# Kernel optimization log

Hardware: AMD Instinct MI355X
Metric: run time of the kernel (lower is better)

## Reference

```python
import jax, jax.numpy as jnp
import numpy as np

B, N, S, F = 16384, 1152, 576, 8  # batch, n_sites, n_symm, features
LOG2 = float(np.log(2.0))


def log_cosh(x):
    # numerically stable log(cosh(x)) = |x| + log1p(exp(-2|x|)) - log(2)
    a = jnp.abs(x)
    return a + jnp.log1p(jnp.exp(-2.0 * a)) - LOG2


def setup_inputs() -> dict:
    key = jax.random.key(0)
    ks = iter(jax.random.split(key, 32))
    f32 = jnp.float32
    d = {}
    d['x'] = jax.random.normal(next(ks), (B, N), dtype=f32)
    d['symmetries'] = jax.random.randint(next(ks), (S, N), 0, N, dtype=jnp.int32)
    d['corr0'] = jax.random.randint(next(ks), (576, 4), 0, N, dtype=jnp.int32)
    d['corr1'] = jax.random.randint(next(ks), (576, 4), 0, N, dtype=jnp.int32)
    d['corr2'] = jax.random.randint(next(ks), (24, 24), 0, N, dtype=jnp.int32)
    d['corr3'] = jax.random.randint(next(ks), (24, 24), 0, N, dtype=jnp.int32)
    d['corr0_symm'] = jax.random.randint(next(ks), (S, 576), 0, 576, dtype=jnp.int32)
    d['corr1_symm'] = jax.random.randint(next(ks), (S, 576), 0, 576, dtype=jnp.int32)
    d['corr2_symm'] = jax.random.randint(next(ks), (S, 24), 0, 24, dtype=jnp.int32)
    d['corr3_symm'] = jax.random.randint(next(ks), (S, 24), 0, 24, dtype=jnp.int32)
    std = 0.01
    d['hidden_bias'] = std * jax.random.normal(next(ks), (F,), dtype=f32)
    d['symm_kernel'] = std * jax.random.normal(next(ks), (F, N), dtype=f32)
    d['visible_bias'] = std * jax.random.normal(next(ks), (2,), dtype=f32)
    d['corr0_bias'] = std * jax.random.normal(next(ks), (1,), dtype=f32)
    d['corr0_kernel'] = std * jax.random.normal(next(ks), (F, 576), dtype=f32)
    d['corr1_bias'] = std * jax.random.normal(next(ks), (1,), dtype=f32)
    d['corr1_kernel'] = std * jax.random.normal(next(ks), (F, 576), dtype=f32)
    d['corr2_bias'] = std * jax.random.normal(next(ks), (1,), dtype=f32)
    d['corr2_kernel'] = std * jax.random.normal(next(ks), (F, 24), dtype=f32)
    d['corr3_bias'] = std * jax.random.normal(next(ks), (1,), dtype=f32)
    d['corr3_kernel'] = std * jax.random.normal(next(ks), (F, 24), dtype=f32)
    d['loop0_hidden_bias'] = std * jax.random.normal(next(ks), (F,), dtype=f32)
    d['loop0_kernel'] = std * jax.random.normal(next(ks), (F, 24), dtype=f32)
    d['loop1_hidden_bias'] = std * jax.random.normal(next(ks), (F,), dtype=f32)
    d['loop1_kernel'] = std * jax.random.normal(next(ks), (F, 24), dtype=f32)
    return d


def reference(x, symmetries, corr0, corr1, corr2, corr3,
              corr0_symm, corr1_symm, corr2_symm, corr3_symm,
              hidden_bias, symm_kernel, visible_bias,
              corr0_bias, corr0_kernel, corr1_bias, corr1_kernel,
              corr2_bias, corr2_kernel, corr3_bias, corr3_kernel,
              loop0_hidden_bias, loop0_kernel, loop1_hidden_bias, loop1_kernel):
    n_batch = x.shape[0]
    # symmetrized kernel: (F, S, N)
    K = jnp.take(symm_kernel, symmetries, axis=1)
    theta = jnp.einsum('bn,fsn->bfs', x, K)  # (B, F, S)
    theta = theta + hidden_bias[:, None]
    bias = jnp.sum(x.reshape(n_batch, -1, 2), axis=1) @ visible_bias  # (B,)

    correlators = [corr0, corr1, corr2, corr3]
    corr_symms = [corr0_symm, corr1_symm, corr2_symm, corr3_symm]
    corr_biases = [corr0_bias, corr1_bias, corr2_bias, corr3_bias]
    corr_kernels = [corr0_kernel, corr1_kernel, corr2_kernel, corr3_kernel]

    corr_values = []
    for corr, csym, cb, ck in zip(correlators, corr_symms, corr_biases, corr_kernels):
        ckk = jnp.take(ck, csym, axis=1)               # (F, S, C)
        cv = jnp.take(x, corr, axis=1).prod(axis=2)    # (B, C)
        corr_values.append(cv)
        theta = theta + jnp.einsum('bc,fsc->bfs', cv, ckk)
        bias = bias + cb * jnp.sum(cv, axis=1)

    out = jnp.sum(log_cosh(theta), axis=(1, 2))  # (B,)

    # last two correlators are loop correlators with dedicated hidden units
    loop_params = [(loop0_hidden_bias, loop0_kernel, corr2_symm, corr_values[2]),
                   (loop1_hidden_bias, loop1_kernel, corr3_symm, corr_values[3])]
    for lhb, lk, lsym, lv in loop_params:
        lkk = jnp.take(lk, lsym, axis=1)                      # (F, S, C)
        lt = jnp.einsum('bc,fsc->bfs', lv, lkk) + lhb[:, None]
        out = out + jnp.sum(log_cosh(lt), axis=(1, 2))

    return out + bias
```

## Files before the change

kernel.cpp:

```cpp
#include <hip/hip_runtime.h>
#include <math.h>

#define B_    16384
#define N_    1152
#define KPAD  2560
#define NK32  80
#define KLOOP 256
#define NOUT  4608
#define NT2   18
#define LOG2F_ 0.69314718055994530942f

typedef unsigned short ushort_t;
typedef __attribute__((ext_vector_type(8))) short short8;
typedef __attribute__((ext_vector_type(4))) float floatx4;

__device__ __forceinline__ float log_cosh_f(float t) {
    float a = fabsf(t);
    return a + __logf(1.0f + __expf(-2.0f * a)) - LOG2F_;
}
__device__ __forceinline__ ushort_t bf16_rne(float f) {
    unsigned int u = __float_as_uint(f);
    return (ushort_t)((u + 0x7fffu + ((u >> 16) & 1u)) >> 16);
}
__device__ __forceinline__ float bf16_to_f(ushort_t h) {
    return __uint_as_float(((unsigned int)h) << 16);
}

typedef __attribute__((address_space(1))) const unsigned int guint;
typedef __attribute__((address_space(3))) unsigned int luint;
__device__ __forceinline__ void gload16(const ushort_t* src, ushort_t* dst) {
    __builtin_amdgcn_global_load_lds((guint*)src, (luint*)dst, 16, 0, 0);
}

#define PIPE_WAIT(N) do {                                     \
    asm volatile("s_waitcnt vmcnt(" #N ")" ::: "memory");     \
    __builtin_amdgcn_s_barrier();                             \
    asm volatile("" ::: "memory"); } while (0)

__global__ __launch_bounds__(256) void build_w(
    const int* __restrict__ symm,
    const int* __restrict__ c0s, const int* __restrict__ c1s,
    const int* __restrict__ c2s, const int* __restrict__ c3s,
    const float* __restrict__ sk,
    const float* __restrict__ ck0, const float* __restrict__ ck1,
    const float* __restrict__ ck2, const float* __restrict__ ck3,
    const float* __restrict__ l0k, const float* __restrict__ l1k,
    ushort_t* __restrict__ Wb, ushort_t* __restrict__ LWb)
{
    __shared__ int idx[2352];
    const int s = blockIdx.x;
    const int tid = threadIdx.x;
    for (int i = tid; i < 1152; i += 256) idx[i] = symm[s * N_ + i];
    for (int i = tid; i < 576; i += 256) idx[1152 + i] = c0s[s * 576 + i];
    for (int i = tid; i < 576; i += 256) idx[1728 + i] = c1s[s * 576 + i];
    if (tid < 24) idx[2304 + tid] = c2s[s * 24 + tid];
    else if (tid < 48) idx[2328 + (tid - 24)] = c3s[s * 24 + (tid - 24)];
    __syncthreads();
    for (int f = 0; f < 8; ++f) {
        ushort_t* wr = Wb + (size_t)(s * 8 + f) * KPAD;
        for (int k = tid; k < KPAD; k += 256) {
            ushort_t o;
            if (k < 1152)      o = bf16_rne(sk[f * N_ + idx[k]]);
            else if (k < 1728) o = bf16_rne(ck0[f * 576 + idx[k]]);
            else if (k < 2304) o = bf16_rne(ck1[f * 576 + idx[k]]);
            else if (k < 2448) {
                int q = k - 2304, g = q / 48, c = q - g * 48;
                float w = (c < 24) ? ck2[f * 24 + idx[2304 + c]]
                                   : ck3[f * 24 + idx[2328 + (c - 24)]];
                ushort_t hi = bf16_rne(w);
                o = (g < 2) ? hi : bf16_rne(w - bf16_to_f(hi));
            } else o = 0;
            wr[k] = o;
        }
        ushort_t* lr = LWb + (size_t)(s * 8 + f) * KLOOP;
        for (int k2 = tid; k2 < KLOOP; k2 += 256) {
            int j2 = k2 >> 7, q = k2 & 127;
            ushort_t o = 0;
            if (q < 72) {
                int g = q / 24, c = q - g * 24;
                float w = j2 ? l1k[f * 24 + idx[2328 + c]]
                             : l0k[f * 24 + idx[2304 + c]];
                ushort_t hi = bf16_rne(w);
                o = (g < 2) ? hi : bf16_rne(w - bf16_to_f(hi));
            }
            lr[k2] = o;
        }
    }
}

__global__ __launch_bounds__(256) void build_cv(
    const float* __restrict__ x,
    const int* __restrict__ corr0, const int* __restrict__ corr1,
    const int* __restrict__ corr2, const int* __restrict__ corr3,
    const float* __restrict__ vb,
    const float* __restrict__ cb0, const float* __restrict__ cb1,
    const float* __restrict__ cb2, const float* __restrict__ cb3,
    ushort_t* __restrict__ XA, ushort_t* __restrict__ CVL,
    float* __restrict__ initb)
{
    __shared__ float xs[N_];
    __shared__ float red[256];
    __shared__ float cvhi[48], cvlo[48];
    const int tid = threadIdx.x;
    const int b = blockIdx.x;
    ushort_t* xr = XA + (size_t)b * KPAD;

    float bias = 0.f;
    const float vb0 = vb[0], vb1 = vb[1];
    for (int i = tid; i < N_; i += 256) {
        float v = x[(size_t)b * N_ + i];
        xs[i] = v;
        bias += v * ((i & 1) ? vb1 : vb0);
        xr[i] = bf16_rne(v);
    }
    __syncthreads();
    float s0 = 0.f, s1 = 0.f, s2 = 0.f, s3 = 0.f;
    for (int c = tid; c < 576; c += 256) {
        const int* i0 = corr0 + c * 4;
        float p = xs[i0[0]] * xs[i0[1]] * xs[i0[2]] * xs[i0[3]];
        xr[1152 + c] = bf16_rne(p); s0 += p;
        const int* i1 = corr1 + c * 4;
        float q = xs[i1[0]] * xs[i1[1]] * xs[i1[2]] * xs[i1[3]];
        xr[1728 + c] = bf16_rne(q); s1 += q;
    }
    if (tid < 48) {
        int j2 = tid / 24, c = tid - j2 * 24;
        const int* ii = (j2 ? corr3 : corr2) + c * 24;
        float p = 1.f;
        for (int j = 0; j < 24; ++j) p *= xs[ii[j]];
        float hv = bf16_to_f(bf16_rne(p));
        cvhi[tid] = hv;
        cvlo[tid] = p - hv;
        if (j2) s3 = p; else s2 = p;
    }
    __syncthreads();
    for (int i = tid; i < KPAD - 2304; i += 256) {
        ushort_t o = 0;
        if (i < 144) {
            int g = i / 48, c = i - g * 48;
            o = bf16_rne(g == 1 ? cvlo[c] : cvhi[c]);
        }
        xr[2304 + i] = o;
    }
    ushort_t* cr = CVL + (size_t)b * KLOOP;
    for (int k2 = tid; k2 < KLOOP; k2 += 256) {
        int j2 = k2 >> 7, q = k2 & 127;
        ushort_t o = 0;
        if (q < 72) {
            int g = q / 24, c = q - g * 24;
            o = bf16_rne(g == 1 ? cvlo[j2 * 24 + c] : cvhi[j2 * 24 + c]);
        }
        cr[k2] = o;
    }
    bias += cb0[0] * s0 + cb1[0] * s1 + cb2[0] * s2 + cb3[0] * s3;
    red[tid] = bias;
    __syncthreads();
    for (int off = 128; off; off >>= 1) {
        if (tid < off) red[tid] += red[tid + off];
        __syncthreads();
    }
    if (tid == 0) initb[b] = red[0];
}

__global__ __launch_bounds__(512, 2) void mfma_gemm(
    const ushort_t* __restrict__ XA, const ushort_t* __restrict__ Wb,
    const ushort_t* __restrict__ CVL, const ushort_t* __restrict__ LWb,
    const float* __restrict__ hidden_bias,
    const float* __restrict__ l0hb, const float* __restrict__ l1hb,
    float* __restrict__ partials)
{
    __shared__ __align__(16) ushort_t sh[65536];
    ushort_t* const A0 = sh;                 ushort_t* const Bu0 = sh + 8192;
    ushort_t* const A1 = sh + 16384;         ushort_t* const Bu1 = sh + 24576;
    ushort_t* const A2 = sh + 32768;         ushort_t* const Bu2 = sh + 40960;
    ushort_t* const A3 = sh + 49152;         ushort_t* const Bu3 = sh + 57344;

    const int tid = threadIdx.x;
    const int l = tid & 63, w = tid >> 6;
    const int wm = w >> 2, wn = w & 3;
    const int lrow = l & 15, lg = l >> 4;
    const int srow = l >> 2;
    const int sgr8 = ((l & 3) ^ (srow & 3)) * 8;

    const int bid = blockIdx.x;
    const int swz = (bid & 7) * 144 + (bid >> 3);
    const int nt = swz % NT2, bt = swz / NT2;
    const int n0 = nt * 256, b0 = bt * 256;

    const ushort_t* XAb  = XA  + (size_t)b0 * KPAD;
    const ushort_t* Wbb  = Wb  + (size_t)n0 * KPAD;
    const ushort_t* CVb  = CVL + (size_t)b0 * KLOOP;
    const ushort_t* LWbb = LWb + (size_t)n0 * KLOOP;

    floatx4 acc[8][4];

    auto STG = [&](const ushort_t* g, int stride, int kg, ushort_t* lbase) {
#pragma unroll
        for (int i = 0; i < 2; ++i) {
            const int r0 = i * 128 + w * 16;
            gload16(g + (size_t)(r0 + srow) * stride + kg + sgr8,
                    lbase + r0 * 32);
        }
    };

    const int ga = (lg ^ (lrow & 3)) * 8;
    const int abase = (wm * 128 + lrow) * 32 + ga;
    const int bbase = (wn * 64 + lrow) * 32 + ga;

    auto TILE = [&](const ushort_t* Ab, const ushort_t* Bb,
                    int kgn, ushort_t* An, ushort_t* Bn, bool doStage) {
        short8 af[4], af2[4], bfr[4];
#pragma unroll
        for (int mi = 0; mi < 4; ++mi)
            af[mi] = *(const short8*)(Ab + abase + mi * 512);
#pragma unroll
        for (int ni = 0; ni < 4; ++ni)
            bfr[ni] = *(const short8*)(Bb + bbase + ni * 512);
        if (doStage) { STG(XAb, KPAD, kgn, An); STG(Wbb, KPAD, kgn, Bn); }
        asm volatile("" ::: "memory");
        __builtin_amdgcn_s_setprio(1);
#pragma unroll
        for (int mi = 0; mi < 4; ++mi)
#pragma unroll
            for (int ni = 0; ni < 4; ++ni)
                acc[mi][ni] = __builtin_amdgcn_mfma_f32_16x16x32_bf16(
                    af[mi], bfr[ni], acc[mi][ni], 0, 0, 0);
        __builtin_amdgcn_s_setprio(0);
#pragma unroll
        for (int mi = 0; mi < 4; ++mi)
            af2[mi] = *(const short8*)(Ab + abase + 2048 + mi * 512);
        __builtin_amdgcn_s_setprio(1);
#pragma unroll
        for (int mi = 0; mi < 4; ++mi)
#pragma unroll
            for (int ni = 0; ni < 4; ++ni)
                acc[mi + 4][ni] = __builtin_amdgcn_mfma_f32_16x16x32_bf16(
                    af2[mi], bfr[ni], acc[mi + 4][ni], 0, 0, 0);
        __builtin_amdgcn_s_setprio(0);
    };

#pragma unroll
    for (int mi = 0; mi < 8; ++mi)
#pragma unroll
        for (int ni = 0; ni < 4; ++ni) acc[mi][ni] = (floatx4){0.f, 0.f, 0.f, 0.f};

    STG(XAb, KPAD, 0, A0);  STG(Wbb, KPAD, 0, Bu0);
    STG(XAb, KPAD, 32, A1); STG(Wbb, KPAD, 32, Bu1);
    STG(XAb, KPAD, 64, A2); STG(Wbb, KPAD, 64, Bu2);
#pragma unroll 1
    for (int tt = 0; tt < 19; ++tt) {
        const int t = tt * 4;
        PIPE_WAIT(8); TILE(A0, Bu0, (t + 3) * 32, A3, Bu3, true);
        PIPE_WAIT(8); TILE(A1, Bu1, (t + 4) * 32, A0, Bu0, true);
        PIPE_WAIT(8); TILE(A2, Bu2, (t + 5) * 32, A1, Bu1, true);
        PIPE_WAIT(8); TILE(A3, Bu3, (t + 6) * 32, A2, Bu2, true);
    }
    PIPE_WAIT(8); TILE(A0, Bu0, 79 * 32, A3, Bu3, true);
    PIPE_WAIT(8); TILE(A1, Bu1, 0, A0, Bu0, false);
    PIPE_WAIT(4); TILE(A2, Bu2, 0, A0, Bu0, false);
    PIPE_WAIT(0); TILE(A3, Bu3, 0, A0, Bu0, false);

    float rs[32];
    {
        const float hbv = hidden_bias[l & 7];
#pragma unroll
        for (int mi = 0; mi < 8; ++mi)
#pragma unroll
            for (int reg = 0; reg < 4; ++reg) {
                float t = 0.f;
#pragma unroll
                for (int ni = 0; ni < 4; ++ni)
                    t += log_cosh_f(acc[mi][ni][reg] + hbv);
                rs[mi * 4 + reg] = t;
            }
    }

#pragma unroll 1
    for (int j2 = 0; j2 < 2; ++j2) {
#pragma unroll
        for (int mi = 0; mi < 8; ++mi)
#pragma unroll
            for (int ni = 0; ni < 4; ++ni) acc[mi][ni] = (floatx4){0.f, 0.f, 0.f, 0.f};
        __syncthreads();
        STG(CVb, KLOOP, j2 * 128 +  0, A0); STG(LWbb, KLOOP, j2 * 128 +  0, Bu0);
        STG(CVb, KLOOP, j2 * 128 + 32, A1); STG(LWbb, KLOOP, j2 * 128 + 32, Bu1);
        STG(CVb, KLOOP, j2 * 128 + 64, A2); STG(LWbb, KLOOP, j2 * 128 + 64, Bu2);
        STG(CVb, KLOOP, j2 * 128 + 96, A3); STG(LWbb, KLOOP, j2 * 128 + 96, Bu3);
        __syncthreads();
        TILE(A0, Bu0, 0, A0, Bu0, false);
        TILE(A1, Bu1, 0, A0, Bu0, false);
        TILE(A2, Bu2, 0, A0, Bu0, false);
        TILE(A3, Bu3, 0, A0, Bu0, false);
        const float lbv = (j2 ? l1hb : l0hb)[l & 7];
#pragma unroll
        for (int mi = 0; mi < 8; ++mi)
#pragma unroll
            for (int reg = 0; reg < 4; ++reg) {
                float t = 0.f;
#pragma unroll
                for (int ni = 0; ni < 4; ++ni)
                    t += log_cosh_f(acc[mi][ni][reg] + lbv);
                rs[mi * 4 + reg] += t;
            }
    }

    __syncthreads();
    float* red = (float*)sh;
#pragma unroll
    for (int mi = 0; mi < 8; ++mi)
#pragma unroll
        for (int reg = 0; reg < 4; ++reg) {
            float v = rs[mi * 4 + reg];
            v += __shfl_xor(v, 1);
            v += __shfl_xor(v, 2);
            v += __shfl_xor(v, 4);
            v += __shfl_xor(v, 8);
            if (lrow == 0)
                red[(wm * 128 + mi * 16 + lg * 4 + reg) * 5 + wn] = v;
        }
    __syncthreads();
    if (tid < 256) {
        float t = red[tid * 5 + 0] + red[tid * 5 + 1] +
                  red[tid * 5 + 2] + red[tid * 5 + 3];
        partials[(size_t)nt * B_ + b0 + tid] = t;
    }
}

__global__ __launch_bounds__(256) void finalize_out(
    const float* __restrict__ initb, const float* __restrict__ partials,
    float* __restrict__ out)
{
    int b = blockIdx.x * 256 + threadIdx.x;
    float s = initb[b];
#pragma unroll
    for (int t = 0; t < NT2; ++t) s += partials[(size_t)t * B_ + b];
    out[b] = s;
}

extern "C" void kernel_launch(void* const* d_in, const int* in_sizes, int n_in,
                              void* d_out, int out_size, void* d_ws, size_t ws_size,
                              hipStream_t stream) {
    const float* x    = (const float*)d_in[0];
    const int* symm   = (const int*)d_in[1];
    const int* corr0  = (const int*)d_in[2];
    const int* corr1  = (const int*)d_in[3];
    const int* corr2  = (const int*)d_in[4];
    const int* corr3  = (const int*)d_in[5];
    const int* c0s    = (const int*)d_in[6];
    const int* c1s    = (const int*)d_in[7];
    const int* c2s    = (const int*)d_in[8];
    const int* c3s    = (const int*)d_in[9];
    const float* hb   = (const float*)d_in[10];
    const float* sk   = (const float*)d_in[11];
    const float* vb   = (const float*)d_in[12];
    const float* cb0  = (const float*)d_in[13];
    const float* ck0  = (const float*)d_in[14];
    const float* cb1  = (const float*)d_in[15];
    const float* ck1  = (const float*)d_in[16];
    const float* cb2  = (const float*)d_in[17];
    const float* ck2  = (const float*)d_in[18];
    const float* cb3  = (const float*)d_in[19];
    const float* ck3  = (const float*)d_in[20];
    const float* l0hb = (const float*)d_in[21];
    const float* l0k  = (const float*)d_in[22];
    const float* l1hb = (const float*)d_in[23];
    const float* l1k  = (const float*)d_in[24];

    ushort_t* wsu = (ushort_t*)d_ws;
    ushort_t* Wb  = wsu;
    ushort_t* XA  = Wb + (size_t)NOUT * KPAD;
    ushort_t* LWb = XA + (size_t)B_ * KPAD;
    ushort_t* CVL = LWb + (size_t)NOUT * KLOOP;
    float* initb    = (float*)(CVL + (size_t)B_ * KLOOP);
    float* partials = initb + B_;

    build_w<<<576, 256, 0, stream>>>(
        symm, c0s, c1s, c2s, c3s, sk, ck0, ck1, ck2, ck3, l0k, l1k, Wb, LWb);
    build_cv<<<B_, 256, 0, stream>>>(
        x, corr0, corr1, corr2, corr3, vb, cb0, cb1, cb2, cb3, XA, CVL, initb);
    mfma_gemm<<<1152, 512, 0, stream>>>(
        XA, Wb, CVL, LWb, hb, l0hb, l1hb, partials);
    finalize_out<<<B_ / 256, 256, 0, stream>>>(initb, partials, (float*)d_out);
}
```

Before: 621.4 us.

## Trim K padding, change LDS swizzle, and split staging around MFMA halves with barriers

Result: no change. 613.2 us (-1.3%).

```diff
diff --git a/kernel.cpp b/kernel.cpp
--- a/kernel.cpp
+++ b/kernel.cpp
@@ -3,8 +3,8 @@
 
 #define B_    16384
 #define N_    1152
-#define KPAD  2560
-#define NK32  80
+#define KPAD  2464
+#define NK32  77
 #define KLOOP 256
 #define NOUT  4608
 #define NT2   18
@@ -180,7 +180,7 @@
     const int wm = w >> 2, wn = w & 3;
     const int lrow = l & 15, lg = l >> 4;
     const int srow = l >> 2;
-    const int sgr8 = ((l & 3) ^ (srow & 3)) * 8;
+    const int sgr8 = ((l & 3) ^ ((srow >> 1) & 3)) * 8;
 
     const int bid = blockIdx.x;
     const int swz = (bid & 7) * 144 + (bid >> 3);
@@ -203,12 +203,12 @@
         }
     };
 
-    const int ga = (lg ^ (lrow & 3)) * 8;
+    const int ga = (lg ^ ((lrow >> 1) & 3)) * 8;
     const int abase = (wm * 128 + lrow) * 32 + ga;
     const int bbase = (wn * 64 + lrow) * 32 + ga;
 
-    auto TILE = [&](const ushort_t* Ab, const ushort_t* Bb,
-                    int kgn, ushort_t* An, ushort_t* Bn, bool doStage) {
+    auto TILE2 = [&](const ushort_t* Ab, const ushort_t* Bb,
+                     int kgn, ushort_t* An, ushort_t* Bn, bool doStage) {
         short8 af[4], af2[4], bfr[4];
 #pragma unroll
         for (int mi = 0; mi < 4; ++mi)
@@ -216,8 +216,11 @@
 #pragma unroll
         for (int ni = 0; ni < 4; ++ni)
             bfr[ni] = *(const short8*)(Bb + bbase + ni * 512);
-        if (doStage) { STG(XAb, KPAD, kgn, An); STG(Wbb, KPAD, kgn, Bn); }
-        asm volatile("" ::: "memory");
+        if (doStage) STG(XAb, KPAD, kgn, An);
+        __builtin_amdgcn_sched_barrier(0);
+        __builtin_amdgcn_s_barrier();
+        asm volatile("s_waitcnt lgkmcnt(0)" ::: "memory");
+        __builtin_amdgcn_sched_barrier(0);
         __builtin_amdgcn_s_setprio(1);
 #pragma unroll
         for (int mi = 0; mi < 4; ++mi)
@@ -226,9 +229,15 @@
                 acc[mi][ni] = __builtin_amdgcn_mfma_f32_16x16x32_bf16(
                     af[mi], bfr[ni], acc[mi][ni], 0, 0, 0);
         __builtin_amdgcn_s_setprio(0);
+        __builtin_amdgcn_s_barrier();
 #pragma unroll
         for (int mi = 0; mi < 4; ++mi)
             af2[mi] = *(const short8*)(Ab + abase + 2048 + mi * 512);
+        if (doStage) STG(Wbb, KPAD, kgn, Bn);
+        __builtin_amdgcn_sched_barrier(0);
+        __builtin_amdgcn_s_barrier();
+        asm volatile("s_waitcnt lgkmcnt(0)" ::: "memory");
+        __builtin_amdgcn_sched_barrier(0);
         __builtin_amdgcn_s_setprio(1);
 #pragma unroll
         for (int mi = 0; mi < 4; ++mi)
@@ -237,6 +246,7 @@
                 acc[mi + 4][ni] = __builtin_amdgcn_mfma_f32_16x16x32_bf16(
                     af2[mi], bfr[ni], acc[mi + 4][ni], 0, 0, 0);
         __builtin_amdgcn_s_setprio(0);
+        __builtin_amdgcn_s_barrier();
     };
 
 #pragma unroll
@@ -248,17 +258,18 @@
     STG(XAb, KPAD, 32, A1); STG(Wbb, KPAD, 32, Bu1);
     STG(XAb, KPAD, 64, A2); STG(Wbb, KPAD, 64, Bu2);
 #pragma unroll 1
-    for (int tt = 0; tt < 19; ++tt) {
+    for (int tt = 0; tt < 18; ++tt) {
         const int t = tt * 4;
-        PIPE_WAIT(8); TILE(A0, Bu0, (t + 3) * 32, A3, Bu3, true);
-        PIPE_WAIT(8); TILE(A1, Bu1, (t + 4) * 32, A0, Bu0, true);
-        PIPE_WAIT(8); TILE(A2, Bu2, (t + 5) * 32, A1, Bu1, true);
-        PIPE_WAIT(8); TILE(A3, Bu3, (t + 6) * 32, A2, Bu2, true);
-    }
-    PIPE_WAIT(8); TILE(A0, Bu0, 79 * 32, A3, Bu3, true);
-    PIPE_WAIT(8); TILE(A1, Bu1, 0, A0, Bu0, false);
-    PIPE_WAIT(4); TILE(A2, Bu2, 0, A0, Bu0, false);
-    PIPE_WAIT(0); TILE(A3, Bu3, 0, A0, Bu0, false);
+        PIPE_WAIT(8); TILE2(A0, Bu0, (t + 3) * 32, A3, Bu3, true);
+        PIPE_WAIT(8); TILE2(A1, Bu1, (t + 4) * 32, A0, Bu0, true);
+        PIPE_WAIT(8); TILE2(A2, Bu2, (t + 5) * 32, A1, Bu1, true);
+        PIPE_WAIT(8); TILE2(A3, Bu3, (t + 6) * 32, A2, Bu2, true);
+    }
+    PIPE_WAIT(8); TILE2(A0, Bu0, 75 * 32, A3, Bu3, true);
+    PIPE_WAIT(8); TILE2(A1, Bu1, 76 * 32, A0, Bu0, true);
+    PIPE_WAIT(8); TILE2(A2, Bu2, 0, A1, Bu1, false);
+    PIPE_WAIT(4); TILE2(A3, Bu3, 0, A1, Bu1, false);
+    PIPE_WAIT(0); TILE2(A0, Bu0, 0, A1, Bu1, false);
 
     float rs[32];
     {
@@ -287,10 +298,10 @@
         STG(CVb, KLOOP, j2 * 128 + 64, A2); STG(LWbb, KLOOP, j2 * 128 + 64, Bu2);
         STG(CVb, KLOOP, j2 * 128 + 96, A3); STG(LWbb, KLOOP, j2 * 128 + 96, Bu3);
         __syncthreads();
-        TILE(A0, Bu0, 0, A0, Bu0, false);
-        TILE(A1, Bu1, 0, A0, Bu0, false);
-        TILE(A2, Bu2, 0, A0, Bu0, false);
-        TILE(A3, Bu3, 0, A0, Bu0, false);
+        TILE2(A0, Bu0, 0, A1, Bu1, false);
+        TILE2(A1, Bu1, 0, A1, Bu1, false);
+        TILE2(A2, Bu2, 0, A1, Bu1, false);
+        TILE2(A3, Bu3, 0, A1, Bu1, false);
         const float lbv = (j2 ? l1hb : l0hb)[l & 7];
 #pragma unroll
         for (int mi = 0; mi < 8; ++mi)
```
